# Kernel tuning notes

Hardware: AMD Instinct MI355X
Metric: run time of the kernel (lower is better)

Reference implementation:

```python
import jax, jax.numpy as jnp
import numpy as np

INPUT_DIM = 256
OUTPUT_DIM = 256
COND_DIM = 128
HIDDEN = 128
BATCH = 512


def setup_inputs() -> dict:
    key = jax.random.key(0)
    ks = jax.random.split(key, 8)
    IO = INPUT_DIM * OUTPUT_DIM
    x = jax.random.normal(ks[0], (BATCH, INPUT_DIM), dtype=jnp.float32)
    cond = jax.random.normal(ks[1], (BATCH, COND_DIM), dtype=jnp.float32)
    base_weight = jax.random.normal(ks[2], (INPUT_DIM, OUTPUT_DIM), dtype=jnp.float32) * 0.01
    base_bias = jnp.zeros((OUTPUT_DIM,), dtype=jnp.float32)
    # hypernet: Linear(cond_dim, hidden) -> ReLU -> Linear(hidden, I*O + O)
    w1 = jax.random.normal(ks[3], (COND_DIM, HIDDEN), dtype=jnp.float32) * (1.0 / np.sqrt(COND_DIM))
    b1 = jnp.zeros((HIDDEN,), dtype=jnp.float32)
    w2 = jax.random.normal(ks[4], (HIDDEN, IO + OUTPUT_DIM), dtype=jnp.float32) * (1.0 / np.sqrt(HIDDEN))
    b2 = jnp.zeros((IO + OUTPUT_DIM,), dtype=jnp.float32)
    return {"x": x, "cond": cond, "base_weight": base_weight, "base_bias": base_bias,
            "w1": w1, "b1": b1, "w2": w2, "b2": b2}


def reference(x, cond, base_weight, base_bias, w1, b1, w2, b2):
    B = x.shape[0]
    IO = INPUT_DIM * OUTPUT_DIM
    # hypernet MLP producing per-sample weight/bias deltas
    h = jax.nn.relu(cond @ w1 + b1)                      # [B, hidden]
    dyn = h @ w2 + b2                                    # [B, I*O + O]
    weight_delta = dyn[:, :IO].reshape(B, INPUT_DIM, OUTPUT_DIM)
    bias_delta = dyn[:, IO:]                             # [B, O]
    W = base_weight[None, :, :] + weight_delta           # [B, I, O]
    b = base_bias[None, :] + bias_delta                  # [B, O]
    out = jnp.einsum('bi,bio->bo', x, W) + b             # per-sample GEMV
    return out
```

## Files before the change

kernel.cpp:

```cpp
#include <hip/hip_runtime.h>
#include <hip/hip_bf16.h>
#include <stdint.h>

#define BATCH    512
#define IN_DIM   256
#define OUT_DIM  256
#define COND_DIM 128
#define HIDDEN   128
#define W2_COLS  65792
#define H_STRIDE 132
#define PLANE_SZ 65536
#define NCHUNKS  34
#define OUT_ELEMS (BATCH * OUT_DIM)
#define SLICE_OFF ((size_t)131 * PLANE_SZ)

typedef __attribute__((ext_vector_type(8))) short bf16x8;
typedef __attribute__((ext_vector_type(4))) float f32x4;

__device__ float          g_h[BATCH * H_STRIDE + 8];
__device__ unsigned short g_hbf[BATCH * HIDDEN];
__device__ unsigned short g_xbf[BATCH * IN_DIM];

static __device__ __forceinline__ unsigned int fbits(float f) {
    union { float f; unsigned int u; } v; v.f = f; return v.u;
}
static __device__ __forceinline__ unsigned short f2bf(float f) {
    return (unsigned short)((fbits(f) + 0x8000u) >> 16);
}
static __device__ __forceinline__ unsigned int pack2(float a, float b) {
    return __builtin_amdgcn_perm(fbits(b) + 0x8000u, fbits(a) + 0x8000u, 0x07060302u);
}
static __device__ __forceinline__ float bf2f(unsigned short u) {
    union { unsigned int u; float f; } v; v.u = ((unsigned int)u) << 16;
    return v.f;
}

__global__ __launch_bounds__(256)
void hyper_prep_kernel(const float* __restrict__ x,
                       const float* __restrict__ cond,
                       const float* __restrict__ base_weight,
                       const float* __restrict__ w1,
                       const float* __restrict__ b1,
                       const float* __restrict__ w2,
                       const float* __restrict__ b2,
                       unsigned short* __restrict__ wt) {
    const int bx = blockIdx.x;
    const int t  = threadIdx.x;
    if (bx < 2088) {
        int p, i0; const float* src; size_t rstride;
        if (bx < 2080) {
            p  = bx >> 4;
            i0 = (bx & 15) * 16;
            src = (p < 128) ? (w2 + (size_t)p * W2_COLS)
                            : (p == 128 ? b2 : base_weight);
            rstride = OUT_DIM;
        } else {
            p  = 130;
            i0 = (bx - 2080) * 16;
            src = w2 + 65536; rstride = W2_COLS;
        }
        const int o = t;
        const float* s = src + (size_t)i0 * rstride + o;
        float f[16];
        #pragma unroll
        for (int j = 0; j < 16; ++j) f[j] = s[(size_t)j * rstride];

        const int nt = o >> 4, kb = i0 >> 5, iq0 = (i0 >> 3) & 3;
        unsigned short* pbase = wt + ((size_t)(p * 16 + nt) * 8 + kb) * 512;
        unsigned int v0[4], v1[4];
        #pragma unroll
        for (int q = 0; q < 4; ++q) {
            v0[q] = pack2(f[q * 2],     f[q * 2 + 1]);
            v1[q] = pack2(f[8 + q * 2], f[8 + q * 2 + 1]);
        }
        *(uint4*)(pbase + ((size_t)(iq0       * 16 + (o & 15))) * 8) = *(uint4*)v0;
        *(uint4*)(pbase + ((size_t)((iq0 + 1) * 16 + (o & 15))) * 8) = *(uint4*)v1;
    } else if (bx < 2104) {
        int base = (bx - 2088) * 8192 + t * 32;
        #pragma unroll
        for (int g = 0; g < 4; ++g) {
            const float4* s4 = (const float4*)(x + base + g * 8);
            float4 a = s4[0], b = s4[1];
            unsigned int vv[4] = { pack2(a.x, a.y), pack2(a.z, a.w),
                                   pack2(b.x, b.y), pack2(b.z, b.w) };
            *(uint4*)(g_xbf + base + g * 8) = *(uint4*)vv;
        }
    } else {
        __shared__ float c[2][COND_DIM];
        int bb = t >> 7, k = t & 127;
        int b  = (bx - 2104) * 2 + bb;
        c[bb][k] = cond[b * COND_DIM + k];
        __syncthreads();
        float acc = b1[k];
        #pragma unroll 8
        for (int i = 0; i < COND_DIM; ++i)
            acc += c[bb][i] * w1[i * HIDDEN + k];
        acc = fmaxf(acc, 0.0f);
        g_h[b * H_STRIDE + k] = acc;
        g_hbf[b * HIDDEN + k] = f2bf(acc);
        if (k < 4) g_h[b * H_STRIDE + 128 + k] = 1.0f;
    }
}

template<int NPL, int NSL>
static __device__ __forceinline__ void run_gemm(
    int p0, const unsigned short* __restrict__ asrc, int astride,
    const unsigned short* __restrict__ wt, unsigned short* __restrict__ slices,
    int chunk, int b0, int o0, int t, const float* __restrict__ h_s)
{
    const int lane = t & 63, wave = t >> 6;
    const int wm = wave >> 1, wn = wave & 1;
    const int qg = lane >> 4, ncol = lane & 15;

    bf16x8 xf[NSL][2][2];
    #pragma unroll
    for (int sl = 0; sl < NSL; ++sl)
        #pragma unroll
        for (int ks = 0; ks < 2; ++ks)
            #pragma unroll
            for (int mf = 0; mf < 2; ++mf)
                xf[sl][ks][mf] = *(const bf16x8*)(asrc
                    + (size_t)(b0 + wm * 32 + mf * 16 + ncol) * astride
                    + sl * 64 + ks * 32 + qg * 8);

    const unsigned short* fb = wt
        + ((size_t)(p0 * 16 + (o0 >> 4) + wn * 2) * 8) * 512 + (size_t)lane * 8;

    f32x4 acc[2][2] = {};

    #pragma unroll
    for (int pl = 0; pl < NPL; ++pl) {
        bf16x8 bfr[NSL][2][2];
        #pragma unroll
        for (int sl = 0; sl < NSL; ++sl)
            #pragma unroll
            for (int ks = 0; ks < 2; ++ks)
                #pragma unroll
                for (int nf = 0; nf < 2; ++nf)
                    bfr[sl][ks][nf] = *(const bf16x8*)(fb + (size_t)pl * PLANE_SZ
                        + (size_t)(nf * 8 + sl * 2 + ks) * 512);

        float hv[2][4];
        #pragma unroll
        for (int mf = 0; mf < 2; ++mf)
            #pragma unroll
            for (int r = 0; r < 4; ++r)
                hv[mf][r] = h_s[(wm * 32 + mf * 16 + qg * 4 + r) * 4 + pl];

        f32x4 pacc[2][2] = {};
        #pragma unroll
        for (int sl = 0; sl < NSL; ++sl)
            #pragma unroll
            for (int ks = 0; ks < 2; ++ks)
                #pragma unroll
                for (int mf = 0; mf < 2; ++mf)
                    #pragma unroll
                    for (int nf = 0; nf < 2; ++nf)
                        pacc[mf][nf] = __builtin_amdgcn_mfma_f32_16x16x32_bf16(
                            xf[sl][ks][mf], bfr[sl][ks][nf], pacc[mf][nf], 0, 0, 0);

        #pragma unroll
        for (int mf = 0; mf < 2; ++mf)
            #pragma unroll
            for (int nf = 0; nf < 2; ++nf)
                #pragma unroll
                for (int r = 0; r < 4; ++r)
                    acc[mf][nf][r] += hv[mf][r] * pacc[mf][nf][r];
    }

    unsigned short* slice = slices + (size_t)chunk * OUT_ELEMS;
    #pragma unroll
    for (int mf = 0; mf < 2; ++mf)
        #pragma unroll
        for (int nf = 0; nf < 2; ++nf)
            #pragma unroll
            for (int r = 0; r < 4; ++r) {
                int row = b0 + wm * 32 + mf * 16 + qg * 4 + r;
                int col = o0 + wn * 32 + nf * 16 + ncol;
                slice[(size_t)row * OUT_DIM + col] = f2bf(acc[mf][nf][r]);
            }
}

__global__ __launch_bounds__(256, 2)
void hyper_main_kernel(const unsigned short* __restrict__ wt,
                       unsigned short* __restrict__ slices) {
    __shared__ float h_s[256];

    const int bx    = blockIdx.x;
    const int chunk = bx >> 5;
    const int rem   = bx & 31;
    const int b0    = (rem >> 2) * 64;
    const int o0    = (rem & 3) * 64;
    const int t     = threadIdx.x;

    const int p0 = (chunk < 32) ? chunk * 4 : (chunk == 32 ? 128 : 130);

    h_s[t] = g_h[(b0 + (t >> 2)) * H_STRIDE + p0 + (t & 3)];
    __syncthreads();

    if (chunk < 32)
        run_gemm<4, 4>(p0, g_xbf, IN_DIM, wt, slices, chunk, b0, o0, t, h_s);
    else if (chunk == 32)
        run_gemm<2, 4>(p0, g_xbf, IN_DIM, wt, slices, chunk, b0, o0, t, h_s);
    else
        run_gemm<1, 2>(p0, g_hbf, HIDDEN, wt, slices, chunk, b0, o0, t, h_s);
}

__global__ void hyper_reduce_kernel(const unsigned short* __restrict__ slices,
                                    const float* __restrict__ base_bias,
                                    const float* __restrict__ b2,
                                    float* __restrict__ out) {
    int i = blockIdx.x * 256 + threadIdx.x;
    int o = (i & 63) * 4;
    float4 bb = *(const float4*)(base_bias + o);
    float4 c2 = *(const float4*)(b2 + 65536 + o);
    float4 a;
    a.x = bb.x + c2.x; a.y = bb.y + c2.y; a.z = bb.z + c2.z; a.w = bb.w + c2.w;
    #pragma unroll
    for (int c = 0; c < NCHUNKS; ++c) {
        ushort4 v = *(const ushort4*)(slices + (size_t)c * OUT_ELEMS + (size_t)i * 4);
        a.x += bf2f(v.x); a.y += bf2f(v.y); a.z += bf2f(v.z); a.w += bf2f(v.w);
    }
    ((float4*)out)[i] = a;
}

extern "C" void kernel_launch(void* const* d_in, const int* in_sizes, int n_in,
                              void* d_out, int out_size, void* d_ws, size_t ws_size,
                              hipStream_t stream) {
    const float* x           = (const float*)d_in[0];
    const float* cond        = (const float*)d_in[1];
    const float* base_weight = (const float*)d_in[2];
    const float* base_bias   = (const float*)d_in[3];
    const float* w1          = (const float*)d_in[4];
    const float* b1          = (const float*)d_in[5];
    const float* w2          = (const float*)d_in[6];
    const float* b2          = (const float*)d_in[7];
    float* out = (float*)d_out;
    unsigned short* ws = (unsigned short*)d_ws;

    hyper_prep_kernel<<<2360, 256, 0, stream>>>(x, cond, base_weight, w1, b1, w2, b2, ws);
    hyper_main_kernel<<<NCHUNKS * 32, 256, 0, stream>>>(ws, ws + SLICE_OFF);
    hyper_reduce_kernel<<<OUT_ELEMS / 4 / 256, 256, 0, stream>>>(ws + SLICE_OFF, base_bias, b2, out);
}
```

Baseline: 129.0 us.

## Fuse split-K reduction into main kernel via last-block atomic counter

Removes the separate reduce kernel launch. Each main-kernel block bumps a per-tile atomic counter after writing its bf16 partial slice, and the last of the 34 chunk blocks for that output tile sums all slices plus biases and writes the output. Counters are zeroed in the prep kernel. This saves one launch and its gap, but serializes the reduction onto a few last blocks (32 tiles of 256 threads) and adds fences and atomics.

```diff
diff --git a/kernel.cpp b/kernel.cpp
--- a/kernel.cpp
+++ b/kernel.cpp
@@ -46,6 +46,10 @@
                        unsigned short* __restrict__ wt) {
     const int bx = blockIdx.x;
     const int t  = threadIdx.x;
+    if (bx == 0 && t < 32) {
+        int* counters = (int*)(wt + SLICE_OFF + (size_t)NCHUNKS * OUT_ELEMS);
+        counters[t] = 0;
+    }
     if (bx < 2088) {
         int p, i0; const float* src; size_t rstride;
         if (bx < 2080) {
@@ -85,7 +89,7 @@
                                    pack2(b.x, b.y), pack2(b.z, b.w) };
             *(uint4*)(g_xbf + base + g * 8) = *(uint4*)vv;
         }
-    } else {
+    } else if (bx >= 2104) {
         __shared__ float c[2][COND_DIM];
         int bb = t >> 7, k = t & 127;
         int b  = (bx - 2104) * 2 + bb;
@@ -183,8 +187,12 @@
 
 __global__ __launch_bounds__(256, 2)
 void hyper_main_kernel(const unsigned short* __restrict__ wt,
-                       unsigned short* __restrict__ slices) {
+                       unsigned short* __restrict__ slices,
+                       const float* __restrict__ base_bias,
+                       const float* __restrict__ b2,
+                       float* __restrict__ out) {
     __shared__ float h_s[256];
+    __shared__ int s_last;
 
     const int bx    = blockIdx.x;
     const int chunk = bx >> 5;
@@ -204,24 +212,43 @@
         run_gemm<2, 4>(p0, g_xbf, IN_DIM, wt, slices, chunk, b0, o0, t, h_s);
     else
         run_gemm<1, 2>(p0, g_hbf, HIDDEN, wt, slices, chunk, b0, o0, t, h_s);
-}
-
-__global__ void hyper_reduce_kernel(const unsigned short* __restrict__ slices,
-                                    const float* __restrict__ base_bias,
-                                    const float* __restrict__ b2,
-                                    float* __restrict__ out) {
-    int i = blockIdx.x * 256 + threadIdx.x;
-    int o = (i & 63) * 4;
-    float4 bb = *(const float4*)(base_bias + o);
-    float4 c2 = *(const float4*)(b2 + 65536 + o);
-    float4 a;
-    a.x = bb.x + c2.x; a.y = bb.y + c2.y; a.z = bb.z + c2.z; a.w = bb.w + c2.w;
-    #pragma unroll
+
+    __threadfence();
+    if (t == 0) {
+        int* counters = (int*)(slices + (size_t)NCHUNKS * OUT_ELEMS);
+        s_last = (atomicAdd(&counters[rem], 1) == NCHUNKS - 1);
+    }
+    __syncthreads();
+    if (!s_last) return;
+    __threadfence();
+
+    const int r  = t >> 2;
+    const int c0 = (t & 3) * 16;
+    float a[16];
+    {
+        const float* bb = base_bias + o0 + c0;
+        const float* cb = b2 + 65536 + o0 + c0;
+        #pragma unroll
+        for (int j = 0; j < 16; ++j) a[j] = bb[j] + cb[j];
+    }
+    #pragma unroll 4
     for (int c = 0; c < NCHUNKS; ++c) {
-        ushort4 v = *(const ushort4*)(slices + (size_t)c * OUT_ELEMS + (size_t)i * 4);
-        a.x += bf2f(v.x); a.y += bf2f(v.y); a.z += bf2f(v.z); a.w += bf2f(v.w);
-    }
-    ((float4*)out)[i] = a;
+        const unsigned short* sp = slices + (size_t)c * OUT_ELEMS
+            + (size_t)(b0 + r) * OUT_DIM + o0 + c0;
+        uint4 v0 = *(const uint4*)sp;
+        uint4 v1 = *(const uint4*)(sp + 8);
+        const unsigned short* u0 = (const unsigned short*)&v0;
+        const unsigned short* u1 = (const unsigned short*)&v1;
+        #pragma unroll
+        for (int j = 0; j < 8; ++j) a[j]     += bf2f(u0[j]);
+        #pragma unroll
+        for (int j = 0; j < 8; ++j) a[8 + j] += bf2f(u1[j]);
+    }
+    float* op = out + (size_t)(b0 + r) * OUT_DIM + o0 + c0;
+    #pragma unroll
+    for (int q = 0; q < 4; ++q)
+        *(float4*)(op + q * 4) = (float4){a[q * 4], a[q * 4 + 1],
+                                          a[q * 4 + 2], a[q * 4 + 3]};
 }
 
 extern "C" void kernel_launch(void* const* d_in, const int* in_sizes, int n_in,
@@ -239,6 +266,5 @@
     unsigned short* ws = (unsigned short*)d_ws;
 
     hyper_prep_kernel<<<2360, 256, 0, stream>>>(x, cond, base_weight, w1, b1, w2, b2, ws);
-    hyper_main_kernel<<<NCHUNKS * 32, 256, 0, stream>>>(ws, ws + SLICE_OFF);
-    hyper_reduce_kernel<<<OUT_ELEMS / 4 / 256, 256, 0, stream>>>(ws + SLICE_OFF, base_bias, b2, out);
-}
+    hyper_main_kernel<<<NCHUNKS * 32, 256, 0, stream>>>(ws, ws + SLICE_OFF, base_bias, b2, out);
+}
```

New measurement: 259.1 us. +101.0%, slower.

## Software-pipeline weight loads with a three-stage register ring and raise occupancy

Applied to the files above, without the earlier changes.

Restructures the per-plane GEMM loop into a flattened stage loop over (plane, slice), prefetching weight fragments two stages ahead into a three-slot register ring instead of loading a whole plane's fragments at once. This lowers peak register use for B fragments and is meant to overlap global loads with MFMA work. Launch bounds are raised to target three blocks per CU, which adds occupancy but risks register spills under the tighter budget.

```diff
diff --git a/kernel.cpp b/kernel.cpp
--- a/kernel.cpp
+++ b/kernel.cpp
@@ -126,46 +126,60 @@
     const unsigned short* fb = wt
         + ((size_t)(p0 * 16 + (o0 >> 4) + wn * 2) * 8) * 512 + (size_t)lane * 8;
 
+    constexpr int NST = NPL * NSL;
+    bf16x8 bb[3][2][2];
+
+    auto loadB = [&](int s, int ring) {
+        const int pl = s / NSL, sl = s % NSL;
+        #pragma unroll
+        for (int ks = 0; ks < 2; ++ks)
+            #pragma unroll
+            for (int nf = 0; nf < 2; ++nf)
+                bb[ring][ks][nf] = *(const bf16x8*)(fb + (size_t)pl * PLANE_SZ
+                    + (size_t)(nf * 8 + sl * 2 + ks) * 512);
+    };
+
+    loadB(0, 0);
+    if (NST > 1) loadB(1, 1);
+
     f32x4 acc[2][2] = {};
-
-    #pragma unroll
-    for (int pl = 0; pl < NPL; ++pl) {
-        bf16x8 bfr[NSL][2][2];
-        #pragma unroll
-        for (int sl = 0; sl < NSL; ++sl)
-            #pragma unroll
-            for (int ks = 0; ks < 2; ++ks)
+    f32x4 pacc[2][2];
+    float hv[2][4];
+
+    #pragma unroll
+    for (int s = 0; s < NST; ++s) {
+        const int pl = s / NSL, sl = s % NSL, ring = s % 3;
+        if (s + 2 < NST) loadB(s + 2, (s + 2) % 3);
+
+        if (sl == 0) {
+            #pragma unroll
+            for (int mf = 0; mf < 2; ++mf)
+                #pragma unroll
+                for (int r = 0; r < 4; ++r)
+                    hv[mf][r] = h_s[(wm * 32 + mf * 16 + qg * 4 + r) * 4 + pl];
+        }
+
+        #pragma unroll
+        for (int ks = 0; ks < 2; ++ks)
+            #pragma unroll
+            for (int mf = 0; mf < 2; ++mf)
+                #pragma unroll
+                for (int nf = 0; nf < 2; ++nf) {
+                    f32x4 c = (sl == 0 && ks == 0) ? (f32x4){0.f, 0.f, 0.f, 0.f}
+                                                   : pacc[mf][nf];
+                    pacc[mf][nf] = __builtin_amdgcn_mfma_f32_16x16x32_bf16(
+                        xf[sl][ks][mf], bb[ring][ks][nf], c, 0, 0, 0);
+                }
+
+        if (sl == NSL - 1) {
+            #pragma unroll
+            for (int mf = 0; mf < 2; ++mf)
                 #pragma unroll
                 for (int nf = 0; nf < 2; ++nf)
-                    bfr[sl][ks][nf] = *(const bf16x8*)(fb + (size_t)pl * PLANE_SZ
-                        + (size_t)(nf * 8 + sl * 2 + ks) * 512);
-
-        float hv[2][4];
-        #pragma unroll
-        for (int mf = 0; mf < 2; ++mf)
-            #pragma unroll
-            for (int r = 0; r < 4; ++r)
-                hv[mf][r] = h_s[(wm * 32 + mf * 16 + qg * 4 + r) * 4 + pl];
-
-        f32x4 pacc[2][2] = {};
-        #pragma unroll
-        for (int sl = 0; sl < NSL; ++sl)
-            #pragma unroll
-            for (int ks = 0; ks < 2; ++ks)
-                #pragma unroll
-                for (int mf = 0; mf < 2; ++mf)
                     #pragma unroll
-                    for (int nf = 0; nf < 2; ++nf)
-                        pacc[mf][nf] = __builtin_amdgcn_mfma_f32_16x16x32_bf16(
-                            xf[sl][ks][mf], bfr[sl][ks][nf], pacc[mf][nf], 0, 0, 0);
-
-        #pragma unroll
-        for (int mf = 0; mf < 2; ++mf)
-            #pragma unroll
-            for (int nf = 0; nf < 2; ++nf)
-                #pragma unroll
-                for (int r = 0; r < 4; ++r)
-                    acc[mf][nf][r] += hv[mf][r] * pacc[mf][nf][r];
+                    for (int r = 0; r < 4; ++r)
+                        acc[mf][nf][r] += hv[mf][r] * pacc[mf][nf][r];
+        }
     }
 
     unsigned short* slice = slices + (size_t)chunk * OUT_ELEMS;
@@ -181,7 +195,7 @@
             }
 }
 
-__global__ __launch_bounds__(256, 2)
+__global__ __launch_bounds__(256, 3)
 void hyper_main_kernel(const unsigned short* __restrict__ wt,
                        unsigned short* __restrict__ slices) {
     __shared__ float h_s[256];
```

Measured after the change: 126.7 us. About the same (-1.7%).
